# Optimization experiments

Measured on AMD Instinct MI355X. Metric: run time of the kernel, lower is better.

## Reference

```python
import jax, jax.numpy as jnp
import numpy as np

N_NODES = 20000
N_EDGES = 320000
DIMS = [256, 256, 128, 64]  # input_dim, hidden_dims...
EPS = 1e-5


def gcn_conv(x, w, b, src, dst, n):
    # PyG GCNConv: linear first, then symmetric-normalized aggregation with self-loops
    x = x @ w  # [N, out]
    loops = jnp.arange(n, dtype=src.dtype)
    src2 = jnp.concatenate([src, loops])
    dst2 = jnp.concatenate([dst, loops])
    deg = jax.ops.segment_sum(jnp.ones_like(dst2, dtype=x.dtype), dst2, num_segments=n)
    dinv = jnp.where(deg > 0, deg ** -0.5, 0.0)
    norm = dinv[src2] * dinv[dst2]  # [E+N]
    msg = x[src2] * norm[:, None]   # gathered, scaled messages
    out = jax.ops.segment_sum(msg, dst2, num_segments=n)
    return out + b


def graph_norm(x, w, b, a):
    # PyG GraphNorm over a single graph: per-feature mean/var across nodes
    mean = jnp.mean(x, axis=0)
    centered = x - a * mean
    var = jnp.mean(centered * centered, axis=0)
    return w * centered * jax.lax.rsqrt(var + EPS) + b


def layer_norm(x, w, b):
    mean = jnp.mean(x, axis=-1, keepdims=True)
    var = jnp.mean((x - mean) ** 2, axis=-1, keepdims=True)
    return (x - mean) * jax.lax.rsqrt(var + EPS) * w + b


def setup_inputs() -> dict:
    key = jax.random.key(0)
    ks = jax.random.split(key, 32)
    inp = {}
    inp["x"] = jax.random.normal(ks[0], (N_NODES, DIMS[0]), dtype=jnp.float32)
    inp["edge_index"] = jax.random.randint(ks[1], (2, N_EDGES), 0, N_NODES, dtype=jnp.int32)
    ki = 2
    for i in range(3):
        fin, fout = DIMS[i], DIMS[i + 1]
        s = 1.0 / np.sqrt(fin)
        inp[f"w{i}"] = jax.random.uniform(ks[ki], (fin, fout), jnp.float32, -s, s); ki += 1
        inp[f"b{i}"] = jnp.zeros((fout,), jnp.float32)
        inp[f"gn{i}_w"] = jnp.ones((fout,), jnp.float32)
        inp[f"gn{i}_b"] = jnp.zeros((fout,), jnp.float32)
        inp[f"gn{i}_a"] = jnp.ones((fout,), jnp.float32)
    h = DIMS[-1]
    s = 1.0 / np.sqrt(3 * h)
    inp["wc1"] = jax.random.uniform(ks[ki], (3 * h, h), jnp.float32, -s, s); ki += 1
    inp["bc1"] = jnp.zeros((h,), jnp.float32)
    inp["ln_w"] = jnp.ones((h,), jnp.float32)
    inp["ln_b"] = jnp.zeros((h,), jnp.float32)
    s = 1.0 / np.sqrt(h)
    inp["wc2"] = jax.random.uniform(ks[ki], (h, 2), jnp.float32, -s, s); ki += 1
    inp["bc2"] = jnp.zeros((2,), jnp.float32)
    return inp


def reference(x, edge_index,
              w0, b0, gn0_w, gn0_b, gn0_a,
              w1, b1, gn1_w, gn1_b, gn1_a,
              w2, b2, gn2_w, gn2_b, gn2_a,
              wc1, bc1, ln_w, ln_b, wc2, bc2):
    src, dst = edge_index[0], edge_index[1]
    n = x.shape[0]
    params = [(w0, b0, gn0_w, gn0_b, gn0_a),
              (w1, b1, gn1_w, gn1_b, gn1_a),
              (w2, b2, gn2_w, gn2_b, gn2_a)]
    for (w, b, gw, gb, ga) in params:
        x_res = x
        x = gcn_conv(x, w, b, src, dst, n)
        x = graph_norm(x, gw, gb, ga)
        x = jax.nn.gelu(x, approximate=False)
        # dropout = identity (eval); residual only when shapes match (layer 0)
        if x.shape == x_res.shape:
            x = x + x_res
    # multi-pool over the single graph (batch vector of zeros): mean | max | sum
    pooled = jnp.concatenate([jnp.mean(x, axis=0), jnp.max(x, axis=0), jnp.sum(x, axis=0)])[None, :]  # [1, 3h]
    h = pooled @ wc1 + bc1
    h = layer_norm(h, ln_w, ln_b)
    h = jax.nn.gelu(h, approximate=False)
    return h @ wc2 + bc2  # [1, num_classes]
```

## Files before the change

kernel.cpp:

```cpp
#include <hip/hip_runtime.h>
#include <math.h>

#define EPSV 1e-5f
#define MAXB 2560

__device__ __forceinline__ float gelu_f(float x) {
    return 0.5f * x * (1.0f + erff(x * 0.70710678118654752440f));
}

__device__ __forceinline__ float4 f4add(float4 a, float4 b) {
    return make_float4(a.x + b.x, a.y + b.y, a.z + b.z, a.w + b.w);
}

__global__ void deg_kernel(const int* __restrict__ ei, int* __restrict__ deg, int E) {
    int stride = gridDim.x * blockDim.x;
    for (int e = blockIdx.x * blockDim.x + threadIdx.x; e < E; e += stride)
        atomicAdd(&deg[ei[E + e]], 1);
}

__global__ void dinv_kernel(const int* __restrict__ deg, float* __restrict__ dinv, int N) {
    int i = blockIdx.x * blockDim.x + threadIdx.x;
    if (i < N) dinv[i] = rsqrtf((float)(deg[i] + 1));
}

__global__ __launch_bounds__(1024) void scan_kernel(const int* __restrict__ deg,
                                                    int* __restrict__ off, int N) {
    __shared__ int sh[1024];
    int t = threadIdx.x;
    int chunk = (N + 1023) >> 10;
    int b = t * chunk;
    int e = b + chunk; if (e > N) e = N;
    int s = 0;
    for (int i = b; i < e; ++i) s += deg[i];
    sh[t] = s;
    __syncthreads();
    for (int d = 1; d < 1024; d <<= 1) {
        int v = (t >= d) ? sh[t - d] : 0;
        __syncthreads();
        sh[t] += v;
        __syncthreads();
    }
    int run = (t > 0) ? sh[t - 1] : 0;
    for (int i = b; i < e; ++i) { off[i] = run; run += deg[i]; }
    if (t == 1023) off[N] = sh[1023];
}

__global__ void fill_kernel(const int* __restrict__ ei, const int* __restrict__ off,
                            int* __restrict__ fill, int* __restrict__ csr, int E) {
    int stride = gridDim.x * blockDim.x;
    for (int e = blockIdx.x * blockDim.x + threadIdx.x; e < E; e += stride) {
        int d = ei[E + e];
        int p = off[d] + atomicAdd(&fill[d], 1);
        csr[p] = ei[e];
    }
}

__global__ __launch_bounds__(256) void gemm_scale_kernel(
    const float* __restrict__ A, const float* __restrict__ W,
    const float* __restrict__ dinv, float* __restrict__ C,
    int M, int K, int Nc)
{
    __shared__ float As[64][17];
    __shared__ float4 Ws4[16][16];
    const int tid = threadIdx.x;
    const int tx = tid & 15, ty = tid >> 4;
    const int row0 = blockIdx.y * 64, col0 = blockIdx.x * 64;
    float acc[4][4] = {};
    const int ar = tid >> 2, ac4 = (tid & 3) * 4;
    const int wr = tid >> 4, wc4 = (tid & 15) * 4;

    for (int kk = 0; kk < K; kk += 16) {
        float4 av = make_float4(0.f, 0.f, 0.f, 0.f);
        int grow = row0 + ar;
        if (grow < M) av = *(const float4*)(A + (long)grow * K + kk + ac4);
        As[ar][ac4 + 0] = av.x; As[ar][ac4 + 1] = av.y;
        As[ar][ac4 + 2] = av.z; As[ar][ac4 + 3] = av.w;
        Ws4[wr][tid & 15] = *(const float4*)(W + (long)(kk + wr) * Nc + col0 + wc4);
        __syncthreads();
#pragma unroll
        for (int k = 0; k < 16; ++k) {
            float4 b4 = Ws4[k][tx];
            float a0 = As[ty * 4 + 0][k];
            float a1 = As[ty * 4 + 1][k];
            float a2 = As[ty * 4 + 2][k];
            float a3 = As[ty * 4 + 3][k];
            acc[0][0] = fmaf(a0, b4.x, acc[0][0]); acc[0][1] = fmaf(a0, b4.y, acc[0][1]);
            acc[0][2] = fmaf(a0, b4.z, acc[0][2]); acc[0][3] = fmaf(a0, b4.w, acc[0][3]);
            acc[1][0] = fmaf(a1, b4.x, acc[1][0]); acc[1][1] = fmaf(a1, b4.y, acc[1][1]);
            acc[1][2] = fmaf(a1, b4.z, acc[1][2]); acc[1][3] = fmaf(a1, b4.w, acc[1][3]);
            acc[2][0] = fmaf(a2, b4.x, acc[2][0]); acc[2][1] = fmaf(a2, b4.y, acc[2][1]);
            acc[2][2] = fmaf(a2, b4.z, acc[2][2]); acc[2][3] = fmaf(a2, b4.w, acc[2][3]);
            acc[3][0] = fmaf(a3, b4.x, acc[3][0]); acc[3][1] = fmaf(a3, b4.y, acc[3][1]);
            acc[3][2] = fmaf(a3, b4.z, acc[3][2]); acc[3][3] = fmaf(a3, b4.w, acc[3][3]);
        }
        __syncthreads();
    }
#pragma unroll
    for (int i = 0; i < 4; ++i) {
        int grow = row0 + ty * 4 + i;
        if (grow < M) {
            float dv = dinv[grow];
            float4 o = make_float4(acc[i][0] * dv, acc[i][1] * dv, acc[i][2] * dv, acc[i][3] * dv);
            *(float4*)(C + (long)grow * Nc + col0 + tx * 4) = o;
        }
    }
}

template<int F>
__global__ __launch_bounds__(256) void gather_kernel(
    const float* __restrict__ hs, const int* __restrict__ off,
    const int* __restrict__ csr, const float* __restrict__ dinv,
    const float* __restrict__ bias, float* __restrict__ t,
    float* __restrict__ p1, float* __restrict__ p2, int N)
{
    constexpr int LPN = F / 4;
    constexpr int NPB = 256 / LPN;
    const int lane = threadIdx.x % LPN;
    const int slot = threadIdx.x / LPN;
    const float4* hs4 = (const float4*)hs;
    float4* t4 = (float4*)t;
    const float4 bv = ((const float4*)bias)[lane];

    float4 a1 = make_float4(0.f, 0.f, 0.f, 0.f);
    float4 a2 = make_float4(0.f, 0.f, 0.f, 0.f);

    for (int d = blockIdx.x * NPB + slot; d < N; d += gridDim.x * NPB) {
        float4 acc = hs4[(long)d * LPN + lane];
        const int e0 = off[d], e1 = off[d + 1];
        int e = e0;
        for (; e + 8 <= e1; e += 8) {
            int s0 = csr[e + 0], s1 = csr[e + 1], s2 = csr[e + 2], s3 = csr[e + 3];
            int s4 = csr[e + 4], s5 = csr[e + 5], s6 = csr[e + 6], s7 = csr[e + 7];
            float4 v0 = hs4[(long)s0 * LPN + lane];
            float4 v1 = hs4[(long)s1 * LPN + lane];
            float4 v2 = hs4[(long)s2 * LPN + lane];
            float4 v3 = hs4[(long)s3 * LPN + lane];
            float4 v4 = hs4[(long)s4 * LPN + lane];
            float4 v5 = hs4[(long)s5 * LPN + lane];
            float4 v6 = hs4[(long)s6 * LPN + lane];
            float4 v7 = hs4[(long)s7 * LPN + lane];
            float4 u0 = f4add(v0, v1);
            float4 u1 = f4add(v2, v3);
            float4 u2 = f4add(v4, v5);
            float4 u3 = f4add(v6, v7);
            float4 w0 = f4add(u0, u1);
            float4 w1 = f4add(u2, u3);
            acc = f4add(acc, f4add(w0, w1));
        }
        for (; e + 2 <= e1; e += 2) {
            int s0 = csr[e + 0], s1 = csr[e + 1];
            float4 v0 = hs4[(long)s0 * LPN + lane];
            float4 v1 = hs4[(long)s1 * LPN + lane];
            acc = f4add(acc, f4add(v0, v1));
        }
        if (e < e1) {
            int s = csr[e];
            acc = f4add(acc, hs4[(long)s * LPN + lane]);
        }

        float dv = dinv[d];
        float4 o;
        o.x = fmaf(dv, acc.x, bv.x);
        o.y = fmaf(dv, acc.y, bv.y);
        o.z = fmaf(dv, acc.z, bv.z);
        o.w = fmaf(dv, acc.w, bv.w);
        t4[(long)d * LPN + lane] = o;
        a1.x += o.x; a1.y += o.y; a1.z += o.z; a1.w += o.w;
        a2.x += o.x * o.x; a2.y += o.y * o.y; a2.z += o.z * o.z; a2.w += o.w * o.w;
    }

    __shared__ float red[8][256];
    red[0][threadIdx.x] = a1.x; red[1][threadIdx.x] = a1.y;
    red[2][threadIdx.x] = a1.z; red[3][threadIdx.x] = a1.w;
    red[4][threadIdx.x] = a2.x; red[5][threadIdx.x] = a2.y;
    red[6][threadIdx.x] = a2.z; red[7][threadIdx.x] = a2.w;
    __syncthreads();
    if (slot == 0) {
        float sum[8];
#pragma unroll
        for (int k = 0; k < 8; ++k) {
            float s = red[k][lane];
            for (int j = 1; j < NPB; ++j) s += red[k][j * LPN + lane];
            sum[k] = s;
        }
        float4 o1 = make_float4(sum[0], sum[1], sum[2], sum[3]);
        float4 o2 = make_float4(sum[4], sum[5], sum[6], sum[7]);
        ((float4*)p1)[(long)lane * MAXB + blockIdx.x] = o1;
        ((float4*)p2)[(long)lane * MAXB + blockIdx.x] = o2;
    }
}

__global__ __launch_bounds__(256) void statreduce_kernel(
    const float* __restrict__ p1, const float* __restrict__ p2,
    const float* __restrict__ ga,
    float* __restrict__ meanv, float* __restrict__ istdv,
    int nb, int N)
{
    const int c4 = blockIdx.x;
    const float4* p14 = (const float4*)p1 + (long)c4 * MAXB;
    const float4* p24 = (const float4*)p2 + (long)c4 * MAXB;
    float4 a1 = make_float4(0.f, 0.f, 0.f, 0.f);
    float4 a2 = make_float4(0.f, 0.f, 0.f, 0.f);
    for (int r = threadIdx.x; r < nb; r += 256) {
        float4 v1 = p14[r];
        float4 v2 = p24[r];
        a1.x += v1.x; a1.y += v1.y; a1.z += v1.z; a1.w += v1.w;
        a2.x += v2.x; a2.y += v2.y; a2.z += v2.z; a2.w += v2.w;
    }
#pragma unroll
    for (int offv = 32; offv > 0; offv >>= 1) {
        a1.x += __shfl_down(a1.x, offv); a1.y += __shfl_down(a1.y, offv);
        a1.z += __shfl_down(a1.z, offv); a1.w += __shfl_down(a1.w, offv);
        a2.x += __shfl_down(a2.x, offv); a2.y += __shfl_down(a2.y, offv);
        a2.z += __shfl_down(a2.z, offv); a2.w += __shfl_down(a2.w, offv);
    }
    __shared__ float4 sh1[4], sh2[4];
    const int wid = threadIdx.x >> 6;
    if ((threadIdx.x & 63) == 0) { sh1[wid] = a1; sh2[wid] = a2; }
    __syncthreads();
    if (threadIdx.x == 0) {
        float4 t1 = sh1[0], t2 = sh2[0];
        for (int j = 1; j < 4; ++j) {
            float4 u1 = sh1[j], u2 = sh2[j];
            t1.x += u1.x; t1.y += u1.y; t1.z += u1.z; t1.w += u1.w;
            t2.x += u2.x; t2.y += u2.y; t2.z += u2.z; t2.w += u2.w;
        }
        float s1a[4] = { t1.x, t1.y, t1.z, t1.w };
        float s2a[4] = { t2.x, t2.y, t2.z, t2.w };
#pragma unroll
        for (int k = 0; k < 4; ++k) {
            int c = c4 * 4 + k;
            float m = s1a[k] / (float)N;
            float a = ga[c];
            float var = s2a[k] / (float)N - 2.f * a * m * m + a * a * m * m;
            meanv[c] = m;
            istdv[c] = rsqrtf(var + EPSV);
        }
    }
}

__global__ __launch_bounds__(256) void normgelu_kernel(
    const float* __restrict__ t, const float* __restrict__ meanv,
    const float* __restrict__ istdv, const float* __restrict__ gw,
    const float* __restrict__ gb, const float* __restrict__ ga,
    const float* __restrict__ res, float* __restrict__ out,
    int log2f, long total)
{
    long stride = (long)gridDim.x * blockDim.x;
    int fmask = (1 << log2f) - 1;
    for (long idx = (long)blockIdx.x * blockDim.x + threadIdx.x; idx < total; idx += stride) {
        int c = (int)idx & fmask;
        float v = t[idx];
        float y = gw[c] * (v - ga[c] * meanv[c]) * istdv[c] + gb[c];
        y = gelu_f(y);
        if (res) y += res[idx];
        out[idx] = y;
    }
}

__device__ __forceinline__ void atomicMaxFloat(float* addr, float val) {
    unsigned* ua = (unsigned*)addr;
    unsigned old = *ua;
    while (true) {
        float of = __uint_as_float(old);
        if (of >= val) break;
        unsigned assumed = old;
        old = atomicCAS(ua, assumed, __float_as_uint(val));
        if (old == assumed) break;
    }
}

__global__ void initpool_kernel(float* __restrict__ psum, float* __restrict__ pmax) {
    int t = threadIdx.x;
    psum[t] = 0.f;
    pmax[t] = -INFINITY;
}

__global__ __launch_bounds__(256) void colpool_kernel(
    const float* __restrict__ x, float* __restrict__ psum, float* __restrict__ pmax,
    int M, int rowsPerBlock)
{
    int c = threadIdx.x & 63;
    int rl = threadIdx.x >> 6;
    int r0 = blockIdx.x * rowsPerBlock;
    int rend = r0 + rowsPerBlock; if (rend > M) rend = M;
    float a1 = 0.f, am = -INFINITY;
    for (int r = r0 + rl; r < rend; r += 4) {
        float v = x[(long)r * 64 + c];
        a1 += v; am = fmaxf(am, v);
    }
    __shared__ float sh1[256], shm[256];
    sh1[threadIdx.x] = a1; shm[threadIdx.x] = am;
    __syncthreads();
    if (threadIdx.x < 64) {
        for (int j = 1; j < 4; ++j) {
            a1 += sh1[c + j * 64];
            am = fmaxf(am, shm[c + j * 64]);
        }
        atomicAdd(&psum[c], a1);
        atomicMaxFloat(&pmax[c], am);
    }
}

__global__ void head_kernel(const float* __restrict__ psum, const float* __restrict__ pmax,
                            const float* __restrict__ wc1, const float* __restrict__ bc1,
                            const float* __restrict__ lnw, const float* __restrict__ lnb,
                            const float* __restrict__ wc2, const float* __restrict__ bc2,
                            float* __restrict__ out, int M)
{
    __shared__ float p[192];
    int t = threadIdx.x;
    float s = psum[t];
    p[t] = s / (float)M;
    p[64 + t] = pmax[t];
    p[128 + t] = s;
    __syncthreads();
    float h = bc1[t];
    for (int k = 0; k < 192; ++k) h = fmaf(p[k], wc1[k * 64 + t], h);
    float m = h;
    for (int off = 32; off > 0; off >>= 1) m += __shfl_xor(m, off);
    m *= (1.f / 64.f);
    float d = h - m;
    float v = d * d;
    for (int off = 32; off > 0; off >>= 1) v += __shfl_xor(v, off);
    v *= (1.f / 64.f);
    float y = d * rsqrtf(v + EPSV) * lnw[t] + lnb[t];
    y = gelu_f(y);
    float o0 = y * wc2[t * 2 + 0];
    float o1 = y * wc2[t * 2 + 1];
    for (int off = 32; off > 0; off >>= 1) {
        o0 += __shfl_xor(o0, off);
        o1 += __shfl_xor(o1, off);
    }
    if (t == 0) {
        out[0] = o0 + bc2[0];
        out[1] = o1 + bc2[1];
    }
}

extern "C" void kernel_launch(void* const* d_in, const int* in_sizes, int n_in,
                              void* d_out, int out_size, void* d_ws, size_t ws_size,
                              hipStream_t stream)
{
    const float* x    = (const float*)d_in[0];
    const int*   ei   = (const int*)d_in[1];
    const float* w0   = (const float*)d_in[2];
    const float* b0   = (const float*)d_in[3];
    const float* gn0w = (const float*)d_in[4];
    const float* gn0b = (const float*)d_in[5];
    const float* gn0a = (const float*)d_in[6];
    const float* w1   = (const float*)d_in[7];
    const float* b1   = (const float*)d_in[8];
    const float* gn1w = (const float*)d_in[9];
    const float* gn1b = (const float*)d_in[10];
    const float* gn1a = (const float*)d_in[11];
    const float* w2   = (const float*)d_in[12];
    const float* b2   = (const float*)d_in[13];
    const float* gn2w = (const float*)d_in[14];
    const float* gn2b = (const float*)d_in[15];
    const float* gn2a = (const float*)d_in[16];
    const float* wc1  = (const float*)d_in[17];
    const float* bc1  = (const float*)d_in[18];
    const float* lnw  = (const float*)d_in[19];
    const float* lnb  = (const float*)d_in[20];
    const float* wc2  = (const float*)d_in[21];
    const float* bc2  = (const float*)d_in[22];

    const int N = in_sizes[0] / 256;
    const int E = in_sizes[1] / 2;

    float* ws = (float*)d_ws;
    const size_t BIG = (size_t)N * 256;
    float* BUF0  = ws;
    float* BUF1  = ws + BIG;
    float* dinv  = ws + 2 * BIG;
    int*   deg   = (int*)(dinv + N);
    int*   off   = deg + N;
    int*   fill  = off + N + 1;
    int*   csr   = fill + N;
    float* p1    = (float*)(csr + E);
    float* p2    = p1 + (size_t)MAXB * 256;
    float* meanv = p2 + (size_t)MAXB * 256;
    float* istdv = meanv + 256;
    float* psum  = istdv + 256;
    float* pmax  = psum + 64;

    hipMemsetAsync(deg, 0, (size_t)N * sizeof(int), stream);
    hipMemsetAsync(fill, 0, (size_t)N * sizeof(int), stream);
    deg_kernel<<<1024, 256, 0, stream>>>(ei, deg, E);
    dinv_kernel<<<(N + 255) / 256, 256, 0, stream>>>(deg, dinv, N);
    scan_kernel<<<1, 1024, 0, stream>>>(deg, off, N);
    fill_kernel<<<1024, 256, 0, stream>>>(ei, off, fill, csr, E);

    struct Layer {
        const float *w, *b, *gw, *gb, *ga;
        int K, F, lf;
    } L[3] = {
        { w0, b0, gn0w, gn0b, gn0a, 256, 256, 8 },
        { w1, b1, gn1w, gn1b, gn1a, 256, 128, 7 },
        { w2, b2, gn2w, gn2b, gn2a, 128,  64, 6 },
    };
    const float* resb[3] = { x, nullptr, nullptr };

    const float* cur = x;
    for (int li = 0; li < 3; ++li) {
        const int K = L[li].K, F = L[li].F, lf = L[li].lf;
        const long total = (long)N << lf;
        dim3 gg(F / 64, (N + 63) / 64);
        gemm_scale_kernel<<<gg, 256, 0, stream>>>(cur, L[li].w, dinv, BUF0, N, K, F);

        int nb;
        if (F == 256) {
            int npb = 4, groups = (N + npb - 1) / npb;
            nb = groups < MAXB ? groups : MAXB;
            gather_kernel<256><<<nb, 256, 0, stream>>>(BUF0, off, csr, dinv, L[li].b, BUF1, p1, p2, N);
        } else if (F == 128) {
            int npb = 8, groups = (N + npb - 1) / npb;
            nb = groups < MAXB ? groups : MAXB;
            gather_kernel<128><<<nb, 256, 0, stream>>>(BUF0, off, csr, dinv, L[li].b, BUF1, p1, p2, N);
        } else {
            int npb = 16, groups = (N + npb - 1) / npb;
            nb = groups < MAXB ? groups : MAXB;
            gather_kernel<64><<<nb, 256, 0, stream>>>(BUF0, off, csr, dinv, L[li].b, BUF1, p1, p2, N);
        }
        statreduce_kernel<<<F / 4, 256, 0, stream>>>(p1, p2, L[li].ga, meanv, istdv, nb, N);

        long fb = (total + 255) / 256; if (fb > 4096) fb = 4096;
        normgelu_kernel<<<(int)fb, 256, 0, stream>>>(BUF1, meanv, istdv,
                                                     L[li].gw, L[li].gb, L[li].ga,
                                                     resb[li], BUF1, lf, total);
        cur = BUF1;
    }

    initpool_kernel<<<1, 64, 0, stream>>>(psum, pmax);
    colpool_kernel<<<(N + 127) / 128, 256, 0, stream>>>(cur, psum, pmax, N, 128);
    head_kernel<<<1, 64, 0, stream>>>(psum, pmax, wc1, bc1, lnw, lnb, wc2, bc2,
                                      (float*)d_out, N);
}
```

Measured before the change: 333.4 us.

## Split gather feature columns into 64-wide groups mapped across blocks by XCD

Each gather block now handles one 64-column slice of the features for 16 nodes, instead of whole feature rows. Blocks are assigned to column groups by blockIdx mod 8, which lines up with round-robin dispatch over the MI355X's eight XCDs. Each XCD therefore touches only a subset of columns, which shrinks its working set in its own L2. The stats reduction now skips partials that belong to other column groups. In exchange, every node's CSR indices are read once per column group, and the grid is fixed at 2080 blocks.

```diff
diff --git a/kernel.cpp b/kernel.cpp
--- a/kernel.cpp
+++ b/kernel.cpp
@@ -3,6 +3,7 @@
 
 #define EPSV 1e-5f
 #define MAXB 2560
+#define GBLK 2080
 
 __device__ __forceinline__ float gelu_f(float x) {
     return 0.5f * x * (1.0f + erff(x * 0.70710678118654752440f));
@@ -113,49 +114,55 @@
     const float* __restrict__ bias, float* __restrict__ t,
     float* __restrict__ p1, float* __restrict__ p2, int N)
 {
-    constexpr int LPN = F / 4;
-    constexpr int NPB = 256 / LPN;
-    const int lane = threadIdx.x % LPN;
-    const int slot = threadIdx.x / LPN;
+    constexpr int NG  = F / 64;
+    constexpr int LDR = F / 4;
+    constexpr int NPB = 16;
+    const int lane = threadIdx.x & 15;
+    const int slot = threadIdx.x >> 4;
+
+    const int xs    = blockIdx.x & 7;
+    const int g     = xs % NG;
+    const int r     = xs / NG;
+    const int chunk = blockIdx.x >> 3;
+    const int repl  = 8 / NG;
+    const int nPerG = (int)(gridDim.x >> 3) * repl;
+    const int j     = chunk * repl + r;
+
+    const int col4 = g * 16 + lane;
     const float4* hs4 = (const float4*)hs;
     float4* t4 = (float4*)t;
-    const float4 bv = ((const float4*)bias)[lane];
+    const float4 bv = ((const float4*)bias)[col4];
 
     float4 a1 = make_float4(0.f, 0.f, 0.f, 0.f);
     float4 a2 = make_float4(0.f, 0.f, 0.f, 0.f);
 
-    for (int d = blockIdx.x * NPB + slot; d < N; d += gridDim.x * NPB) {
-        float4 acc = hs4[(long)d * LPN + lane];
+    for (int d = j * NPB + slot; d < N; d += nPerG * NPB) {
+        float4 acc = hs4[(long)d * LDR + col4];
         const int e0 = off[d], e1 = off[d + 1];
         int e = e0;
         for (; e + 8 <= e1; e += 8) {
             int s0 = csr[e + 0], s1 = csr[e + 1], s2 = csr[e + 2], s3 = csr[e + 3];
             int s4 = csr[e + 4], s5 = csr[e + 5], s6 = csr[e + 6], s7 = csr[e + 7];
-            float4 v0 = hs4[(long)s0 * LPN + lane];
-            float4 v1 = hs4[(long)s1 * LPN + lane];
-            float4 v2 = hs4[(long)s2 * LPN + lane];
-            float4 v3 = hs4[(long)s3 * LPN + lane];
-            float4 v4 = hs4[(long)s4 * LPN + lane];
-            float4 v5 = hs4[(long)s5 * LPN + lane];
-            float4 v6 = hs4[(long)s6 * LPN + lane];
-            float4 v7 = hs4[(long)s7 * LPN + lane];
+            float4 v0 = hs4[(long)s0 * LDR + col4];
+            float4 v1 = hs4[(long)s1 * LDR + col4];
+            float4 v2 = hs4[(long)s2 * LDR + col4];
+            float4 v3 = hs4[(long)s3 * LDR + col4];
+            float4 v4 = hs4[(long)s4 * LDR + col4];
+            float4 v5 = hs4[(long)s5 * LDR + col4];
+            float4 v6 = hs4[(long)s6 * LDR + col4];
+            float4 v7 = hs4[(long)s7 * LDR + col4];
             float4 u0 = f4add(v0, v1);
             float4 u1 = f4add(v2, v3);
             float4 u2 = f4add(v4, v5);
             float4 u3 = f4add(v6, v7);
-            float4 w0 = f4add(u0, u1);
-            float4 w1 = f4add(u2, u3);
-            acc = f4add(acc, f4add(w0, w1));
+            acc = f4add(acc, f4add(f4add(u0, u1), f4add(u2, u3)));
         }
         for (; e + 2 <= e1; e += 2) {
             int s0 = csr[e + 0], s1 = csr[e + 1];
-            float4 v0 = hs4[(long)s0 * LPN + lane];
-            float4 v1 = hs4[(long)s1 * LPN + lane];
-            acc = f4add(acc, f4add(v0, v1));
+            acc = f4add(acc, f4add(hs4[(long)s0 * LDR + col4], hs4[(long)s1 * LDR + col4]));
         }
         if (e < e1) {
-            int s = csr[e];
-            acc = f4add(acc, hs4[(long)s * LPN + lane]);
+            acc = f4add(acc, hs4[(long)csr[e] * LDR + col4]);
         }
 
         float dv = dinv[d];
@@ -164,7 +171,7 @@
         o.y = fmaf(dv, acc.y, bv.y);
         o.z = fmaf(dv, acc.z, bv.z);
         o.w = fmaf(dv, acc.w, bv.w);
-        t4[(long)d * LPN + lane] = o;
+        t4[(long)d * LDR + col4] = o;
         a1.x += o.x; a1.y += o.y; a1.z += o.z; a1.w += o.w;
         a2.x += o.x * o.x; a2.y += o.y * o.y; a2.z += o.z * o.z; a2.w += o.w * o.w;
     }
@@ -180,13 +187,11 @@
 #pragma unroll
         for (int k = 0; k < 8; ++k) {
             float s = red[k][lane];
-            for (int j = 1; j < NPB; ++j) s += red[k][j * LPN + lane];
+            for (int jj = 1; jj < NPB; ++jj) s += red[k][jj * 16 + lane];
             sum[k] = s;
         }
-        float4 o1 = make_float4(sum[0], sum[1], sum[2], sum[3]);
-        float4 o2 = make_float4(sum[4], sum[5], sum[6], sum[7]);
-        ((float4*)p1)[(long)lane * MAXB + blockIdx.x] = o1;
-        ((float4*)p2)[(long)lane * MAXB + blockIdx.x] = o2;
+        ((float4*)p1)[(long)col4 * MAXB + blockIdx.x] = make_float4(sum[0], sum[1], sum[2], sum[3]);
+        ((float4*)p2)[(long)col4 * MAXB + blockIdx.x] = make_float4(sum[4], sum[5], sum[6], sum[7]);
     }
 }
 
@@ -194,14 +199,16 @@
     const float* __restrict__ p1, const float* __restrict__ p2,
     const float* __restrict__ ga,
     float* __restrict__ meanv, float* __restrict__ istdv,
-    int nb, int N)
+    int nb, int N, int NG)
 {
     const int c4 = blockIdx.x;
+    const int g = (c4 >> 4) % NG;
     const float4* p14 = (const float4*)p1 + (long)c4 * MAXB;
     const float4* p24 = (const float4*)p2 + (long)c4 * MAXB;
     float4 a1 = make_float4(0.f, 0.f, 0.f, 0.f);
     float4 a2 = make_float4(0.f, 0.f, 0.f, 0.f);
     for (int r = threadIdx.x; r < nb; r += 256) {
+        if (((r & 7) % NG) != g) continue;
         float4 v1 = p14[r];
         float4 v2 = p24[r];
         a1.x += v1.x; a1.y += v1.y; a1.z += v1.z; a1.w += v1.w;
@@ -220,8 +227,8 @@
     __syncthreads();
     if (threadIdx.x == 0) {
         float4 t1 = sh1[0], t2 = sh2[0];
-        for (int j = 1; j < 4; ++j) {
-            float4 u1 = sh1[j], u2 = sh2[j];
+        for (int jj = 1; jj < 4; ++jj) {
+            float4 u1 = sh1[jj], u2 = sh2[jj];
             t1.x += u1.x; t1.y += u1.y; t1.z += u1.z; t1.w += u1.w;
             t2.x += u2.x; t2.y += u2.y; t2.z += u2.z; t2.w += u2.w;
         }
@@ -409,21 +416,14 @@
         dim3 gg(F / 64, (N + 63) / 64);
         gemm_scale_kernel<<<gg, 256, 0, stream>>>(cur, L[li].w, dinv, BUF0, N, K, F);
 
-        int nb;
         if (F == 256) {
-            int npb = 4, groups = (N + npb - 1) / npb;
-            nb = groups < MAXB ? groups : MAXB;
-            gather_kernel<256><<<nb, 256, 0, stream>>>(BUF0, off, csr, dinv, L[li].b, BUF1, p1, p2, N);
+            gather_kernel<256><<<GBLK, 256, 0, stream>>>(BUF0, off, csr, dinv, L[li].b, BUF1, p1, p2, N);
         } else if (F == 128) {
-            int npb = 8, groups = (N + npb - 1) / npb;
-            nb = groups < MAXB ? groups : MAXB;
-            gather_kernel<128><<<nb, 256, 0, stream>>>(BUF0, off, csr, dinv, L[li].b, BUF1, p1, p2, N);
+            gather_kernel<128><<<GBLK, 256, 0, stream>>>(BUF0, off, csr, dinv, L[li].b, BUF1, p1, p2, N);
         } else {
-            int npb = 16, groups = (N + npb - 1) / npb;
-            nb = groups < MAXB ? groups : MAXB;
-            gather_kernel<64><<<nb, 256, 0, stream>>>(BUF0, off, csr, dinv, L[li].b, BUF1, p1, p2, N);
-        }
-        statreduce_kernel<<<F / 4, 256, 0, stream>>>(p1, p2, L[li].ga, meanv, istdv, nb, N);
+            gather_kernel<64><<<GBLK, 256, 0, stream>>>(BUF0, off, csr, dinv, L[li].b, BUF1, p1, p2, N);
+        }
+        statreduce_kernel<<<F / 4, 256, 0, stream>>>(p1, p2, L[li].ga, meanv, istdv, GBLK, N, F / 64);
 
         long fb = (total + 255) / 256; if (fb > 4096) fb = 4096;
         normgelu_kernel<<<(int)fb, 256, 0, stream>>>(BUF1, meanv, istdv,
```

Result: faster. 318.4 us (-4.5%).
